# Kernel optimization log

Measured on AMD Instinct MI355X. Metric: run time of the kernel, lower is better.

The kernel has to match this reference:

```python
import jax, jax.numpy as jnp
import numpy as np


def squash(s, axis):
    # torch: mag_sq/(1+mag_sq) * s/mag, reduced over the given axis
    mag_sq = jnp.sum(s * s, axis=axis, keepdims=True)
    mag = jnp.sqrt(mag_sq)
    return mag_sq / (1.0 + mag_sq) * (s / mag)


def setup_inputs() -> dict:
    key = jax.random.key(0)
    ks = jax.random.split(key, 13)
    B, D_IN, H = 64, 227989, 512
    NU, CO, K = 8, 8, 8            # num_primary_units, conv out channels, kernel
    L = (H - K) // 2 + 1           # 253
    PSIZE = NU * 0 + CO * L        # 2024 per primary capsule
    NOUT, USIZE = 4, 64            # output capsules
    f32 = jnp.float32
    return {
        "x": jax.random.normal(ks[0], (B, D_IN), f32),
        "fc_w": jax.random.normal(ks[1], (H, D_IN), f32) * 0.002,
        "fc_b": jax.random.normal(ks[2], (H,), f32) * 0.01,
        "conv_w": jax.random.normal(ks[3], (NU, CO, 1, K), f32) * 0.1,
        "conv_b": jax.random.normal(ks[4], (NU, CO), f32) * 0.01,
        "W_dig": jax.random.normal(ks[5], (PSIZE, NOUT, USIZE, NU), f32) * 0.05,
        "fc2_w1": jax.random.normal(ks[6], (128, 256), f32) * 0.05,
        "fc2_b1": jnp.zeros((128,), f32),
        "fc2_w2": jax.random.normal(ks[7], (64, 128), f32) * 0.08,
        "fc2_b2": jnp.zeros((64,), f32),
        "fc2_w3": jax.random.normal(ks[8], (2, 64), f32) * 0.1,
        "fc2_b3": jnp.zeros((2,), f32),
    }


def reference(x, fc_w, fc_b, conv_w, conv_b, W_dig,
              fc2_w1, fc2_b1, fc2_w2, fc2_b2, fc2_w3, fc2_b3):
    B = x.shape[0]
    # fc + ReLU (nn.ReLU overwrote the LeakyReLU attribute)
    sdae = jnp.maximum(x @ fc_w.T + fc_b, 0.0)[:, None, :]   # [B,1,512]

    # primary capsules (no routing): 8 ConvUnits fused into one conv
    NU, CO, _, K = conv_w.shape
    rhs = conv_w.reshape(NU * CO, 1, K)
    u = jax.lax.conv_general_dilated(sdae, rhs, (2,), 'VALID',
                                     dimension_numbers=('NCH', 'OIH', 'NCH'))
    u = u + conv_b.reshape(1, NU * CO, 1)                     # [B,64,253]
    u = u.reshape(B, NU, -1)                                  # [B,8,2024]
    u = squash(u, 2)

    # digits capsule: dynamic routing, 3 iterations
    xt = jnp.swapaxes(u, 1, 2)                                # [B,2024,8]
    u_hat = jnp.einsum('cjdi,bci->bcjd', W_dig, xt)           # [B,2024,4,64]
    C, J = W_dig.shape[0], W_dig.shape[1]
    b_ij = jnp.zeros((C, J), u_hat.dtype)
    for _ in range(3):
        c_ij = jax.nn.softmax(b_ij, axis=0)                   # softmax over in_channels
        s_j = jnp.einsum('cj,bcjd->bjd', c_ij, u_hat)         # [B,4,64]
        v_j = squash(s_j, 1)                                  # torch squashes dim=2 = capsule dim j
        b_ij = b_ij + jnp.mean(jnp.einsum('bcjd,bjd->bcj', u_hat, v_j), axis=0)

    caps = v_j.reshape(B, -1)                                 # [B,256]
    lrelu = lambda z: jnp.where(z >= 0, z, 0.01 * z)          # LeakyReLU; dropout in eval = identity
    h = lrelu(caps @ fc2_w1.T + fc2_b1)
    h = lrelu(h @ fc2_w2.T + fc2_b2)
    logits = h @ fc2_w3.T + fc2_b3                            # [B,2]
    return (logits, sdae)
```

## Files before the change

### kernel.cpp

```cpp
#include <hip/hip_runtime.h>
#include <hip/hip_bf16.h>

typedef __attribute__((ext_vector_type(8))) short s16x8;
typedef __attribute__((ext_vector_type(4))) float f32x4;

#define D_IN 227989
#define KSPLIT 128
#define KC 1792
#define NSTEPS 28
#define APITCH 68
#define BUFSZ (128 * APITCH)

__device__ __forceinline__ unsigned short f2bf(float f) {
    unsigned int u = __float_as_uint(f);
    u = (u + 0x7FFFu + ((u >> 16) & 1u)) >> 16;
    return (unsigned short)u;
}

__device__ __forceinline__ void gload_lds(const float* g, float* l) {
    __builtin_amdgcn_global_load_lds(
        (const __attribute__((address_space(1))) void*)g,
        (__attribute__((address_space(3))) void*)l, 4, 0, 0);
}

__device__ __forceinline__ s16x8 cvt8(const float* p) {
    f32x4 lo = *(const f32x4*)p;
    f32x4 hi = *(const f32x4*)(p + 4);
    s16x8 r;
    r[0] = (short)f2bf(lo[0]); r[1] = (short)f2bf(lo[1]);
    r[2] = (short)f2bf(lo[2]); r[3] = (short)f2bf(lo[3]);
    r[4] = (short)f2bf(hi[0]); r[5] = (short)f2bf(hi[1]);
    r[6] = (short)f2bf(hi[2]); r[7] = (short)f2bf(hi[3]);
    return r;
}

__device__ __forceinline__ void stage_tile(const float* ga, const float* gb,
                                           float* lbase, int wid) {
    float* la = lbase + (wid * 16) * APITCH;
    float* lb = lbase + (64 + wid * 16) * APITCH;
    #pragma unroll
    for (int i = 0; i < 16; ++i) {
        gload_lds(ga + (long)i * D_IN, la + i * APITCH);
        gload_lds(gb + (long)i * D_IN, lb + i * APITCH);
    }
}

__device__ __forceinline__ void compute_tile(const float* base, int wid,
                                             int frow, int koct, f32x4* acc) {
    const float* B = base + (64 + wid * 16 + frow) * APITCH + koct * 8;
    const s16x8 b0 = cvt8(B);
    const s16x8 b1 = cvt8(B + 32);
    const float* A = base + frow * APITCH + koct * 8;
    #pragma unroll
    for (int m = 0; m < 4; ++m) {
        const s16x8 a0 = cvt8(A + m * 16 * APITCH);
        const s16x8 a1 = cvt8(A + m * 16 * APITCH + 32);
        acc[m] = __builtin_amdgcn_mfma_f32_16x16x32_bf16(a0, b0, acc[m], 0, 0, 0);
        acc[m] = __builtin_amdgcn_mfma_f32_16x16x32_bf16(a1, b1, acc[m], 0, 0, 0);
    }
}

__global__ __launch_bounds__(256) void k_fc_gemm(const float* __restrict__ x,
                                                 const float* __restrict__ w,
                                                 float* __restrict__ part) {
    __shared__ __align__(16) float lds[2 * BUFSZ];
    const int t = threadIdx.x;
    const int wid = t >> 6, lane = t & 63;
    const int frow = lane & 15, koct = lane >> 4;
    const int bx = blockIdx.x;
    const int nt = bx & 7, ks = bx >> 3;
    const long k0 = (long)ks * KC;

    const float* ga = x + (long)(wid * 16) * D_IN + k0 + lane;
    const float* gb = w + (long)(nt * 64 + wid * 16) * D_IN + k0 + lane;

    f32x4 acc[4] = {};

    if (k0 + KC <= D_IN) {
        stage_tile(ga, gb, lds, wid);
        int cur = 0;
        #pragma unroll 1
        for (int s = 0; s < NSTEPS - 1; ++s) {
            stage_tile(ga + (s + 1) * 64, gb + (s + 1) * 64,
                       lds + (cur ^ 1) * BUFSZ, wid);
            asm volatile("s_waitcnt vmcnt(32)" ::: "memory");
            __builtin_amdgcn_s_barrier();
            asm volatile("" ::: "memory");
            compute_tile(lds + cur * BUFSZ, wid, frow, koct, acc);
            asm volatile("" ::: "memory");
            __builtin_amdgcn_s_barrier();
            cur ^= 1;
        }
        asm volatile("s_waitcnt vmcnt(0)" ::: "memory");
        __builtin_amdgcn_s_barrier();
        asm volatile("" ::: "memory");
        compute_tile(lds + cur * BUFSZ, wid, frow, koct, acc);
    } else {
        const int rem = (int)(D_IN - k0);
        const int nst = (rem + 63) >> 6;
        for (int s = 0; s < nst; ++s) {
            const int kk = s * 64 + lane;
            const bool ok = kk < rem;
            float va[16], vb[16];
            #pragma unroll
            for (int i = 0; i < 16; ++i) {
                va[i] = ok ? ga[(long)i * D_IN + s * 64] : 0.0f;
                vb[i] = ok ? gb[(long)i * D_IN + s * 64] : 0.0f;
            }
            __syncthreads();
            #pragma unroll
            for (int i = 0; i < 16; ++i) {
                lds[(wid * 16 + i) * APITCH + lane] = va[i];
                lds[(64 + wid * 16 + i) * APITCH + lane] = vb[i];
            }
            __syncthreads();
            compute_tile(lds, wid, frow, koct, acc);
        }
    }

    const int g16 = nt * 4 + wid;
    float* __restrict__ po = part + ((long)(g16 * KSPLIT + ks) << 10);
    #pragma unroll
    for (int m = 0; m < 4; ++m)
        #pragma unroll
        for (int r = 0; r < 4; ++r)
            po[(m * 16 + koct * 4 + r) * 16 + frow] = acc[m][r];
}

__global__ __launch_bounds__(256) void k_fc_reduce(const float* __restrict__ part,
                                                   const float* __restrict__ bias,
                                                   float* __restrict__ sdae) {
    const int i = blockIdx.x * 256 + threadIdx.x;
    const int m = i >> 9, n = i & 511;
    const int nt = n >> 4, nl = n & 15;
    const float* p = part + ((long)nt * KSPLIT << 10) + m * 16 + nl;
    float s = 0.f;
    #pragma unroll 4
    for (int ks = 0; ks < KSPLIT; ++ks) s += p[(long)ks << 10];
    s += bias[n];
    sdae[i] = fmaxf(s, 0.0f);
}

__global__ __launch_bounds__(256) void k_conv_squash(const float* __restrict__ sdae,
                                                     const float* __restrict__ cw,
                                                     const float* __restrict__ cb,
                                                     float* __restrict__ xt) {
    __shared__ float row_s[512];
    __shared__ float us[64 * 253];
    __shared__ float part[256];
    __shared__ float scale_s[8];
    const int b = blockIdx.x, t = threadIdx.x;
    row_s[t] = sdae[b * 512 + t];
    row_s[t + 256] = sdae[b * 512 + t + 256];
    __syncthreads();
    const int ch = t >> 2, lq = t & 3;
    float wreg[8];
    #pragma unroll
    for (int k = 0; k < 8; ++k) wreg[k] = cw[ch * 8 + k];
    const float bias = cb[ch];
    const int l0 = lq * 64;
    const int l1 = (lq == 3) ? 253 : (l0 + 64);
    float ssq = 0.f;
    for (int l = l0; l < l1; ++l) {
        float v = bias;
        #pragma unroll
        for (int k = 0; k < 8; ++k) v += row_s[2 * l + k] * wreg[k];
        us[ch * 253 + l] = v;
        ssq += v * v;
    }
    part[t] = ssq;
    __syncthreads();
    if (t < 8) {
        float s = 0.f;
        for (int i = 0; i < 32; ++i) s += part[t * 32 + i];
        scale_s[t] = sqrtf(s) / (1.0f + s);
    }
    __syncthreads();
    const int nu = ch >> 3, co = ch & 7;
    const float sc = scale_s[nu];
    for (int l = l0; l < l1; ++l)
        xt[(long)b * 16192 + (long)(co * 253 + l) * 8 + nu] = us[ch * 253 + l] * sc;
}

template <int UNIFORM>
__global__ __launch_bounds__(256) void k_route_s(const float* __restrict__ W,
                                                 const float* __restrict__ xt,
                                                 const float* __restrict__ cij,
                                                 float* __restrict__ spart) {
    __shared__ __align__(16) float xs[64 * 132];
    __shared__ __align__(16) float wsh[16 * 768];
    const int bx = blockIdx.x;
    const int j = bx >> 6, cs = bx & 63;
    const int c0 = cs * 32;
    const int t = threadIdx.x;
    const int bg = t >> 4, dg = t & 15;
    float acc[4][4] = {};
    #pragma unroll 1
    for (int cc0 = 0; cc0 < 32; cc0 += 16) {
        {
            const int bb = t >> 2, p = t & 3;
            const float* src = xt + (long)bb * 16192 + (long)(c0 + cc0) * 8 + p * 32;
            float* dst = &xs[bb * 132 + p * 32];
            if (c0 + cc0 + 16 <= 2024) {
                #pragma unroll
                for (int e = 0; e < 32; e += 4) *(f32x4*)(dst + e) = *(const f32x4*)(src + e);
            } else {
                for (int e = 0; e < 32; ++e) {
                    int cidx = c0 + cc0 + ((p * 32 + e) >> 3);
                    dst[e] = (cidx < 2024) ? src[e] : 0.0f;
                }
            }
        }
        {
            const int ccs = t >> 4, dp = t & 15;
            const int c = c0 + cc0 + ccs;
            float* o = &wsh[ccs * 768 + dp * 48];
            if (c < 2024) {
                const float sc = UNIFORM ? (1.0f / 2024.0f) : cij[j * 2024 + c];
                const float* wsrc = W + (long)c * 2048 + j * 512 + dp * 32;
                #pragma unroll
                for (int dd = 0; dd < 4; ++dd) {
                    f32x4 w0 = *(const f32x4*)(wsrc + dd * 8);
                    f32x4 w1 = *(const f32x4*)(wsrc + dd * 8 + 4);
                    float* od = o + dd * 12;
                    od[0] = w0[0] * sc; od[1] = w0[1] * sc; od[2] = w0[2] * sc; od[3] = w0[3] * sc;
                    od[4] = w1[0] * sc; od[5] = w1[1] * sc; od[6] = w1[2] * sc; od[7] = w1[3] * sc;
                }
            } else {
                #pragma unroll
                for (int dd = 0; dd < 4; ++dd) {
                    float* od = o + dd * 12;
                    #pragma unroll
                    for (int e = 0; e < 8; ++e) od[e] = 0.0f;
                }
            }
        }
        __syncthreads();
        int ccN = 2024 - c0 - cc0;
        if (ccN > 16) ccN = 16;
        for (int cc = 0; cc < ccN; ++cc) {
            float xv[4][8], wv[4][8];
            #pragma unroll
            for (int bb = 0; bb < 4; ++bb) {
                *(f32x4*)&xv[bb][0] = *(const f32x4*)&xs[(bg * 4 + bb) * 132 + cc * 8];
                *(f32x4*)&xv[bb][4] = *(const f32x4*)&xs[(bg * 4 + bb) * 132 + cc * 8 + 4];
            }
            #pragma unroll
            for (int dd = 0; dd < 4; ++dd) {
                const int d = dg + dd * 16;
                *(f32x4*)&wv[dd][0] = *(const f32x4*)&wsh[cc * 768 + d * 12];
                *(f32x4*)&wv[dd][4] = *(const f32x4*)&wsh[cc * 768 + d * 12 + 4];
            }
            #pragma unroll
            for (int bb = 0; bb < 4; ++bb)
                #pragma unroll
                for (int dd = 0; dd < 4; ++dd)
                    #pragma unroll
                    for (int i = 0; i < 8; ++i)
                        acc[bb][dd] += xv[bb][i] * wv[dd][i];
        }
        __syncthreads();
    }
    float* sp = spart + ((long)bx << 12);
    #pragma unroll
    for (int bb = 0; bb < 4; ++bb)
        #pragma unroll
        for (int dd = 0; dd < 4; ++dd)
            sp[(bg * 4 + bb) * 64 + dg + dd * 16] = acc[bb][dd];
}

__global__ __launch_bounds__(256) void k_route_v(const float* __restrict__ spart,
                                                 float* __restrict__ v) {
    __shared__ float sj[256];
    const int b = blockIdx.x, t = threadIdx.x;
    const int d = t & 63;
    const int j = t >> 6;
    float s = 0.f;
    #pragma unroll 4
    for (int cs = 0; cs < 64; ++cs)
        s += spart[((long)(j * 64 + cs) << 12) + (b << 6) + d];
    sj[t] = s;
    __syncthreads();
    float msq = 0.f;
    #pragma unroll
    for (int q = 0; q < 4; ++q) { float z = sj[q * 64 + d]; msq += z * z; }
    v[(b << 8) + t] = s * (sqrtf(msq) / (1.0f + msq));
}

template <int ADD>
__global__ __launch_bounds__(256) void k_route_a(const float* __restrict__ W,
                                                 const float* __restrict__ xt,
                                                 const float* __restrict__ v,
                                                 float* __restrict__ bij) {
    __shared__ __align__(16) float xts[64 * 68];
    __shared__ __align__(16) float vts[4 * 4360];
    __shared__ float red[256];
    const int c0 = blockIdx.x * 8;
    const int t = threadIdx.x;
    for (int idx = t; idx < 16384; idx += 256) {
        int b = idx >> 8, r = idx & 255;
        vts[(r >> 6) * 4360 + (r & 63) * 68 + b] = v[idx];
    }
    for (int idx = t; idx < 4096; idx += 256) {
        int b = idx >> 6, r = idx & 63;
        xts[r * 68 + b] = xt[(long)b * 16192 + (long)c0 * 8 + r];
    }
    __syncthreads();
    const int cc = t >> 5, jj = (t >> 3) & 3, p = t & 7;
    float Wreg[8][8];
    const float* wb = W + (long)(c0 + cc) * 2048 + jj * 512;
    #pragma unroll
    for (int dd = 0; dd < 8; ++dd) {
        const int d = p + dd * 8;
        *(f32x4*)&Wreg[dd][0] = *(const f32x4*)(wb + d * 8);
        *(f32x4*)&Wreg[dd][4] = *(const f32x4*)(wb + d * 8 + 4);
    }
    float a0 = 0.f, a1 = 0.f, a2 = 0.f, a3 = 0.f;
    for (int b0 = 0; b0 < 64; b0 += 4) {
        float xq[8][4];
        #pragma unroll
        for (int i = 0; i < 8; ++i)
            *(f32x4*)&xq[i][0] = *(const f32x4*)&xts[(cc * 8 + i) * 68 + b0];
        #pragma unroll
        for (int dd = 0; dd < 8; ++dd) {
            const int d = p + dd * 8;
            f32x4 vq = *(const f32x4*)&vts[jj * 4360 + d * 68 + b0];
            float u0 = 0, u1 = 0, u2 = 0, u3 = 0;
            #pragma unroll
            for (int i = 0; i < 8; ++i) {
                const float wv = Wreg[dd][i];
                u0 += wv * xq[i][0]; u1 += wv * xq[i][1];
                u2 += wv * xq[i][2]; u3 += wv * xq[i][3];
            }
            a0 += u0 * vq[0]; a1 += u1 * vq[1]; a2 += u2 * vq[2]; a3 += u3 * vq[3];
        }
    }
    red[t] = a0 + a1 + a2 + a3;
    __syncthreads();
    if (p == 0) {
        float s = 0.f;
        #pragma unroll
        for (int q2 = 0; q2 < 8; ++q2) s += red[t + q2];
        s *= (1.0f / 64.0f);
        const int idx = (c0 + cc) * 4 + jj;
        bij[idx] = ADD ? (bij[idx] + s) : s;
    }
}

__global__ __launch_bounds__(256) void k_softmax(const float* __restrict__ bij,
                                                 float* __restrict__ cij) {
    __shared__ float red[256];
    const int j = blockIdx.x, t = threadIdx.x;
    float vals[8];
    float m = -1e30f;
    #pragma unroll
    for (int q = 0; q < 8; ++q) {
        const int c = q * 256 + t;
        const float z = (c < 2024) ? bij[c * 4 + j] : -1e30f;
        vals[q] = z;
        m = fmaxf(m, z);
    }
    red[t] = m;
    __syncthreads();
    for (int s = 128; s > 0; s >>= 1) {
        if (t < s) red[t] = fmaxf(red[t], red[t + s]);
        __syncthreads();
    }
    m = red[0];
    __syncthreads();
    float sum = 0.f;
    #pragma unroll
    for (int q = 0; q < 8; ++q) {
        const int c = q * 256 + t;
        const float e = (c < 2024) ? __expf(vals[q] - m) : 0.0f;
        vals[q] = e;
        sum += e;
    }
    red[t] = sum;
    __syncthreads();
    for (int s = 128; s > 0; s >>= 1) {
        if (t < s) red[t] += red[t + s];
        __syncthreads();
    }
    const float inv = 1.0f / red[0];
    #pragma unroll
    for (int q = 0; q < 8; ++q) {
        const int c = q * 256 + t;
        if (c < 2024) cij[j * 2024 + c] = vals[q] * inv;
    }
}

__global__ __launch_bounds__(256) void k_fc2(const float* __restrict__ v,
                                             const float* __restrict__ w1, const float* __restrict__ b1,
                                             const float* __restrict__ w2, const float* __restrict__ b2,
                                             const float* __restrict__ w3, const float* __restrict__ b3,
                                             float* __restrict__ logits) {
    __shared__ float caps[256], h1[128], h2[64];
    const int b = blockIdx.x, t = threadIdx.x;
    caps[t] = v[b * 256 + t];
    __syncthreads();
    if (t < 128) {
        float s = b1[t];
        const float* wr = w1 + t * 256;
        for (int k = 0; k < 256; ++k) s += wr[k] * caps[k];
        h1[t] = (s >= 0.f) ? s : 0.01f * s;
    }
    __syncthreads();
    if (t < 64) {
        float s = b2[t];
        const float* wr = w2 + t * 128;
        for (int k = 0; k < 128; ++k) s += wr[k] * h1[k];
        h2[t] = (s >= 0.f) ? s : 0.01f * s;
    }
    __syncthreads();
    if (t < 2) {
        float s = b3[t];
        const float* wr = w3 + t * 64;
        for (int k = 0; k < 64; ++k) s += wr[k] * h2[k];
        logits[b * 2 + t] = s;
    }
}

extern "C" void kernel_launch(void* const* d_in, const int* in_sizes, int n_in,
                              void* d_out, int out_size, void* d_ws, size_t ws_size,
                              hipStream_t stream) {
    const float* x      = (const float*)d_in[0];
    const float* fc_w   = (const float*)d_in[1];
    const float* fc_b   = (const float*)d_in[2];
    const float* conv_w = (const float*)d_in[3];
    const float* conv_b = (const float*)d_in[4];
    const float* W_dig  = (const float*)d_in[5];
    const float* w1 = (const float*)d_in[6];
    const float* b1 = (const float*)d_in[7];
    const float* w2 = (const float*)d_in[8];
    const float* b2 = (const float*)d_in[9];
    const float* w3 = (const float*)d_in[10];
    const float* b3 = (const float*)d_in[11];

    float* out    = (float*)d_out;
    float* logits = out;
    float* sdae   = out + 128;

    float* ws     = (float*)d_ws;
    float* ws_fc  = ws;
    float* ws_xt  = ws_fc + 4194304;
    float* ws_sp  = ws_xt + 1036288;
    float* ws_v   = ws_sp + 1048576;
    float* ws_bij = ws_v + 16384;
    float* ws_cij = ws_bij + 8096;

    k_fc_gemm<<<1024, 256, 0, stream>>>(x, fc_w, ws_fc);
    k_fc_reduce<<<128, 256, 0, stream>>>(ws_fc, fc_b, sdae);
    k_conv_squash<<<64, 256, 0, stream>>>(sdae, conv_w, conv_b, ws_xt);

    k_route_s<1><<<256, 256, 0, stream>>>(W_dig, ws_xt, ws_cij, ws_sp);
    k_route_v<<<64, 256, 0, stream>>>(ws_sp, ws_v);
    k_route_a<0><<<253, 256, 0, stream>>>(W_dig, ws_xt, ws_v, ws_bij);
    k_softmax<<<4, 256, 0, stream>>>(ws_bij, ws_cij);
    k_route_s<0><<<256, 256, 0, stream>>>(W_dig, ws_xt, ws_cij, ws_sp);
    k_route_v<<<64, 256, 0, stream>>>(ws_sp, ws_v);
    k_route_a<1><<<253, 256, 0, stream>>>(W_dig, ws_xt, ws_v, ws_bij);
    k_softmax<<<4, 256, 0, stream>>>(ws_bij, ws_cij);
    k_route_s<0><<<256, 256, 0, stream>>>(W_dig, ws_xt, ws_cij, ws_sp);
    k_route_v<<<64, 256, 0, stream>>>(ws_sp, ws_v);

    k_fc2<<<64, 256, 0, stream>>>(ws_v, w1, b1, w2, b2, w3, b3, logits);
}
```

Measured before the change: 304.4 us.

## Replace global_load_lds staging with 16-byte register-staged loads and skewed LDS rows

The fc GEMM main loop stops using per-dword global_load_lds and instead loads f32x4 vectors into registers, then writes them to LDS with a register double-buffer (two staging sets ping-ponging across two LDS buffers). Because D_IN is odd, rows are misaligned for 16-byte loads, so each row is shifted by (row&3) with an extra tail vector that fills columns 64..67 of the pitch. Compute reads use the matching per-row offset with scalar element reads, and the tail path writes with the same skew. This is meant to cut the number of memory instructions and improve load efficiency, at the cost of more registers, extra LDS write traffic and unaligned scalar LDS reads in the conversion.

```diff
diff --git a/kernel.cpp b/kernel.cpp
--- a/kernel.cpp
+++ b/kernel.cpp
@@ -17,47 +17,65 @@
     return (unsigned short)u;
 }
 
-__device__ __forceinline__ void gload_lds(const float* g, float* l) {
-    __builtin_amdgcn_global_load_lds(
-        (const __attribute__((address_space(1))) void*)g,
-        (__attribute__((address_space(3))) void*)l, 4, 0, 0);
-}
-
-__device__ __forceinline__ s16x8 cvt8(const float* p) {
-    f32x4 lo = *(const f32x4*)p;
-    f32x4 hi = *(const f32x4*)(p + 4);
+__device__ __forceinline__ s16x8 cvt8u(const float* p) {
     s16x8 r;
-    r[0] = (short)f2bf(lo[0]); r[1] = (short)f2bf(lo[1]);
-    r[2] = (short)f2bf(lo[2]); r[3] = (short)f2bf(lo[3]);
-    r[4] = (short)f2bf(hi[0]); r[5] = (short)f2bf(hi[1]);
-    r[6] = (short)f2bf(hi[2]); r[7] = (short)f2bf(hi[3]);
+    #pragma unroll
+    for (int e = 0; e < 8; ++e) r[e] = (short)f2bf(p[e]);
     return r;
 }
 
-__device__ __forceinline__ void stage_tile(const float* ga, const float* gb,
-                                           float* lbase, int wid) {
-    float* la = lbase + (wid * 16) * APITCH;
-    float* lb = lbase + (64 + wid * 16) * APITCH;
-    #pragma unroll
-    for (int i = 0; i < 16; ++i) {
-        gload_lds(ga + (long)i * D_IN, la + i * APITCH);
-        gload_lds(gb + (long)i * D_IN, lb + i * APITCH);
-    }
-}
-
-__device__ __forceinline__ void compute_tile(const float* base, int wid,
+struct Stg {
+    f32x4 a0, a1, a2, a3, b0, b1, b2, b3, tl;
+};
+
+__device__ __forceinline__ void load_set(Stg& S, const float* pxa, const float* pwa,
+                                         const float* ptl, int lane, int s) {
+    const long o = (long)s * 64;
+    S.a0 = *(const f32x4*)(pxa + o);
+    S.a1 = *(const f32x4*)(pxa + o + 4l * D_IN);
+    S.a2 = *(const f32x4*)(pxa + o + 8l * D_IN);
+    S.a3 = *(const f32x4*)(pxa + o + 12l * D_IN);
+    S.b0 = *(const f32x4*)(pwa + o);
+    S.b1 = *(const f32x4*)(pwa + o + 4l * D_IN);
+    S.b2 = *(const f32x4*)(pwa + o + 8l * D_IN);
+    S.b3 = *(const f32x4*)(pwa + o + 12l * D_IN);
+    if (lane < 32) S.tl = *(const f32x4*)(ptl + o);
+}
+
+__device__ __forceinline__ void write_set(const Stg& S, float* buf,
+                                          int wid, int rr, int ll, int lane) {
+    float* pa = buf + (wid * 16 + rr) * APITCH + ll * 4;
+    *(f32x4*)(pa) = S.a0;
+    *(f32x4*)(pa + 4 * APITCH) = S.a1;
+    *(f32x4*)(pa + 8 * APITCH) = S.a2;
+    *(f32x4*)(pa + 12 * APITCH) = S.a3;
+    float* pb = buf + (64 + wid * 16 + rr) * APITCH + ll * 4;
+    *(f32x4*)(pb) = S.b0;
+    *(f32x4*)(pb + 4 * APITCH) = S.b1;
+    *(f32x4*)(pb + 8 * APITCH) = S.b2;
+    *(f32x4*)(pb + 12 * APITCH) = S.b3;
+    if (lane < 32) {
+        const int lr = (lane < 16) ? (wid * 16 + lane) : (64 + wid * 16 + lane - 16);
+        *(f32x4*)(buf + lr * APITCH + 64) = S.tl;
+    }
+}
+
+__device__ __forceinline__ void compute_tile(const float* buf, int wid,
                                              int frow, int koct, f32x4* acc) {
-    const float* B = base + (64 + wid * 16 + frow) * APITCH + koct * 8;
-    const s16x8 b0 = cvt8(B);
-    const s16x8 b1 = cvt8(B + 32);
-    const float* A = base + frow * APITCH + koct * 8;
+    const int off = (frow & 3) + koct * 8;
+    const float* B = buf + (64 + wid * 16 + frow) * APITCH + off;
+    const s16x8 b0 = cvt8u(B);
+    const s16x8 b1 = cvt8u(B + 32);
     #pragma unroll
     for (int m = 0; m < 4; ++m) {
-        const s16x8 a0 = cvt8(A + m * 16 * APITCH);
-        const s16x8 a1 = cvt8(A + m * 16 * APITCH + 32);
-        acc[m] = __builtin_amdgcn_mfma_f32_16x16x32_bf16(a0, b0, acc[m], 0, 0, 0);
-        acc[m] = __builtin_amdgcn_mfma_f32_16x16x32_bf16(a1, b1, acc[m], 0, 0, 0);
-    }
+        const float* A = buf + (m * 16 + frow) * APITCH + off;
+        acc[m] = __builtin_amdgcn_mfma_f32_16x16x32_bf16(cvt8u(A), b0, acc[m], 0, 0, 0);
+        acc[m] = __builtin_amdgcn_mfma_f32_16x16x32_bf16(cvt8u(A + 32), b1, acc[m], 0, 0, 0);
+    }
+}
+
+__device__ __forceinline__ void bar() {
+    asm volatile("s_waitcnt lgkmcnt(0)\n\ts_barrier" ::: "memory");
 }
 
 __global__ __launch_bounds__(256) void k_fc_gemm(const float* __restrict__ x,
@@ -67,37 +85,47 @@
     const int t = threadIdx.x;
     const int wid = t >> 6, lane = t & 63;
     const int frow = lane & 15, koct = lane >> 4;
+    const int rr = lane >> 4, ll = lane & 15;
     const int bx = blockIdx.x;
     const int nt = bx & 7, ks = bx >> 3;
     const long k0 = (long)ks * KC;
 
-    const float* ga = x + (long)(wid * 16) * D_IN + k0 + lane;
-    const float* gb = w + (long)(nt * 64 + wid * 16) * D_IN + k0 + lane;
+    float* L0 = lds;
+    float* L1 = lds + BUFSZ;
 
     f32x4 acc[4] = {};
 
     if (k0 + KC <= D_IN) {
-        stage_tile(ga, gb, lds, wid);
-        int cur = 0;
+        const float* pxa = x + (long)(wid * 16 + rr) * D_IN + k0 - rr + ll * 4;
+        const float* pwa = w + (long)(nt * 64 + wid * 16 + rr) * D_IN + k0 - rr + ll * 4;
+        const int Lr = lane & 15;
+        const float* ptl = ((lane < 16) ? (x + (long)(wid * 16 + Lr) * D_IN)
+                                        : (w + (long)(nt * 64 + wid * 16 + Lr) * D_IN))
+                           + k0 + 64 - (Lr & 3);
+
+        Stg SA, SB;
+        load_set(SA, pxa, pwa, ptl, lane, 0);
+        load_set(SB, pxa, pwa, ptl, lane, 1);
+        write_set(SA, L0, wid, rr, ll, lane);
+        bar();
         #pragma unroll 1
-        for (int s = 0; s < NSTEPS - 1; ++s) {
-            stage_tile(ga + (s + 1) * 64, gb + (s + 1) * 64,
-                       lds + (cur ^ 1) * BUFSZ, wid);
-            asm volatile("s_waitcnt vmcnt(32)" ::: "memory");
-            __builtin_amdgcn_s_barrier();
-            asm volatile("" ::: "memory");
-            compute_tile(lds + cur * BUFSZ, wid, frow, koct, acc);
-            asm volatile("" ::: "memory");
-            __builtin_amdgcn_s_barrier();
-            cur ^= 1;
-        }
-        asm volatile("s_waitcnt vmcnt(0)" ::: "memory");
-        __builtin_amdgcn_s_barrier();
-        asm volatile("" ::: "memory");
-        compute_tile(lds + cur * BUFSZ, wid, frow, koct, acc);
+        for (int s = 0; s < NSTEPS; s += 2) {
+            if (s + 2 < NSTEPS) load_set(SA, pxa, pwa, ptl, lane, s + 2);
+            write_set(SB, L1, wid, rr, ll, lane);
+            bar();
+            compute_tile(L0, wid, frow, koct, acc);
+            bar();
+            if (s + 3 < NSTEPS) load_set(SB, pxa, pwa, ptl, lane, s + 3);
+            if (s + 2 < NSTEPS) write_set(SA, L0, wid, rr, ll, lane);
+            bar();
+            compute_tile(L1, wid, frow, koct, acc);
+            bar();
+        }
     } else {
         const int rem = (int)(D_IN - k0);
         const int nst = (rem + 63) >> 6;
+        const float* ga = x + (long)(wid * 16) * D_IN + k0 + lane;
+        const float* gb = w + (long)(nt * 64 + wid * 16) * D_IN + k0 + lane;
         for (int s = 0; s < nst; ++s) {
             const int kk = s * 64 + lane;
             const bool ok = kk < rem;
@@ -110,8 +138,8 @@
             __syncthreads();
             #pragma unroll
             for (int i = 0; i < 16; ++i) {
-                lds[(wid * 16 + i) * APITCH + lane] = va[i];
-                lds[(64 + wid * 16 + i) * APITCH + lane] = vb[i];
+                lds[(wid * 16 + i) * APITCH + lane + (i & 3)] = va[i];
+                lds[(64 + wid * 16 + i) * APITCH + lane + (i & 3)] = vb[i];
             }
             __syncthreads();
             compute_tile(lds, wid, frow, koct, acc);
```

After: 318.6 us. +4.6%, slower.

## Deepen FC GEMM LDS pipeline to four buffers and use packed bf16 conversion

Applied to the files above, without the earlier changes.

The main FC GEMM loop now uses four LDS buffers with a prefetch distance of two tiles instead of double buffering. This keeps more global-to-LDS loads in flight and drops the trailing barrier from each iteration. The software fp32-to-bf16 rounding is replaced by the hardware v_cvt_pk_bf16_f32 instruction, which cuts VALU work in the compute step. The larger LDS footprint (about 139 KB per block) likely limits each CU to one resident block, so the deeper per-block pipelining comes at the cost of occupancy.

```diff
diff --git a/kernel.cpp b/kernel.cpp
--- a/kernel.cpp
+++ b/kernel.cpp
@@ -11,10 +11,17 @@
 #define APITCH 68
 #define BUFSZ (128 * APITCH)
 
-__device__ __forceinline__ unsigned short f2bf(float f) {
-    unsigned int u = __float_as_uint(f);
-    u = (u + 0x7FFFu + ((u >> 16) & 1u)) >> 16;
-    return (unsigned short)u;
+__device__ __forceinline__ s16x8 pk2(f32x4 lo, f32x4 hi) {
+    union { int i[4]; s16x8 s; } u;
+    asm("v_cvt_pk_bf16_f32 %0, %1, %2" : "=v"(u.i[0]) : "v"(lo[0]), "v"(lo[1]));
+    asm("v_cvt_pk_bf16_f32 %0, %1, %2" : "=v"(u.i[1]) : "v"(lo[2]), "v"(lo[3]));
+    asm("v_cvt_pk_bf16_f32 %0, %1, %2" : "=v"(u.i[2]) : "v"(hi[0]), "v"(hi[1]));
+    asm("v_cvt_pk_bf16_f32 %0, %1, %2" : "=v"(u.i[3]) : "v"(hi[2]), "v"(hi[3]));
+    return u.s;
+}
+
+__device__ __forceinline__ s16x8 cvt8(const float* p) {
+    return pk2(*(const f32x4*)p, *(const f32x4*)(p + 4));
 }
 
 __device__ __forceinline__ void gload_lds(const float* g, float* l) {
@@ -23,17 +30,6 @@
         (__attribute__((address_space(3))) void*)l, 4, 0, 0);
 }
 
-__device__ __forceinline__ s16x8 cvt8(const float* p) {
-    f32x4 lo = *(const f32x4*)p;
-    f32x4 hi = *(const f32x4*)(p + 4);
-    s16x8 r;
-    r[0] = (short)f2bf(lo[0]); r[1] = (short)f2bf(lo[1]);
-    r[2] = (short)f2bf(lo[2]); r[3] = (short)f2bf(lo[3]);
-    r[4] = (short)f2bf(hi[0]); r[5] = (short)f2bf(hi[1]);
-    r[6] = (short)f2bf(hi[2]); r[7] = (short)f2bf(hi[3]);
-    return r;
-}
-
 __device__ __forceinline__ void stage_tile(const float* ga, const float* gb,
                                            float* lbase, int wid) {
     float* la = lbase + (wid * 16) * APITCH;
@@ -45,12 +41,12 @@
     }
 }
 
-__device__ __forceinline__ void compute_tile(const float* base, int wid,
+__device__ __forceinline__ void compute_tile(const float* buf, int wid,
                                              int frow, int koct, f32x4* acc) {
-    const float* B = base + (64 + wid * 16 + frow) * APITCH + koct * 8;
+    const float* B = buf + (64 + wid * 16 + frow) * APITCH + koct * 8;
     const s16x8 b0 = cvt8(B);
     const s16x8 b1 = cvt8(B + 32);
-    const float* A = base + frow * APITCH + koct * 8;
+    const float* A = buf + frow * APITCH + koct * 8;
     #pragma unroll
     for (int m = 0; m < 4; ++m) {
         const s16x8 a0 = cvt8(A + m * 16 * APITCH);
@@ -63,7 +59,7 @@
 __global__ __launch_bounds__(256) void k_fc_gemm(const float* __restrict__ x,
                                                  const float* __restrict__ w,
                                                  float* __restrict__ part) {
-    __shared__ __align__(16) float lds[2 * BUFSZ];
+    __shared__ __align__(16) float lds[4 * BUFSZ];
     const int t = threadIdx.x;
     const int wid = t >> 6, lane = t & 63;
     const int frow = lane & 15, koct = lane >> 4;
@@ -77,24 +73,20 @@
     f32x4 acc[4] = {};
 
     if (k0 + KC <= D_IN) {
-        stage_tile(ga, gb, lds, wid);
-        int cur = 0;
+        stage_tile(ga, gb, lds + 0 * BUFSZ, wid);
+        stage_tile(ga + 64, gb + 64, lds + 1 * BUFSZ, wid);
         #pragma unroll 1
-        for (int s = 0; s < NSTEPS - 1; ++s) {
-            stage_tile(ga + (s + 1) * 64, gb + (s + 1) * 64,
-                       lds + (cur ^ 1) * BUFSZ, wid);
-            asm volatile("s_waitcnt vmcnt(32)" ::: "memory");
+        for (int s = 0; s < NSTEPS; ++s) {
+            if (s + 2 < NSTEPS)
+                stage_tile(ga + (s + 2) * 64, gb + (s + 2) * 64,
+                           lds + ((s + 2) & 3) * BUFSZ, wid);
+            if (s + 2 < NSTEPS)      asm volatile("s_waitcnt vmcnt(63)" ::: "memory");
+            else if (s + 1 < NSTEPS) asm volatile("s_waitcnt vmcnt(32)" ::: "memory");
+            else                     asm volatile("s_waitcnt vmcnt(0)"  ::: "memory");
             __builtin_amdgcn_s_barrier();
             asm volatile("" ::: "memory");
-            compute_tile(lds + cur * BUFSZ, wid, frow, koct, acc);
-            asm volatile("" ::: "memory");
-            __builtin_amdgcn_s_barrier();
-            cur ^= 1;
-        }
-        asm volatile("s_waitcnt vmcnt(0)" ::: "memory");
-        __builtin_amdgcn_s_barrier();
-        asm volatile("" ::: "memory");
-        compute_tile(lds + cur * BUFSZ, wid, frow, koct, acc);
+            compute_tile(lds + (s & 3) * BUFSZ, wid, frow, koct, acc);
+        }
     } else {
         const int rem = (int)(D_IN - k0);
         const int nst = (rem + 63) >> 6;
```

New measurement: 303.9 us. Within noise of the previous version (-0.2%).
